# Performance work log

Hardware: AMD Instinct MI355X
Metric: run time of the kernel (lower is better)

## Reference

```python
import jax, jax.numpy as jnp
import numpy as np

H = 128   # hidden_size
IN = 4    # input_size
OUT = 4   # linear output dim


def _lstm_layer(x, Wih, Whh, bih, bhh):
    """Single PyTorch-convention LSTM layer (gate order i,f,g,o), batch_first.
    x: [B,T,D] -> hidden states [B,T,H]."""
    B, T, _ = x.shape
    Hd = Whh.shape[1]
    # Precompute input contribution to gates for all timesteps: [B,T,4H]
    xg = jnp.einsum('btd,gd->btg', x, Wih) + bih + bhh
    xg = jnp.swapaxes(xg, 0, 1)  # [T,B,4H] for scan
    h0 = jnp.zeros((B, Hd), x.dtype)
    c0 = jnp.zeros((B, Hd), x.dtype)

    def step(carry, gx):
        h, c = carry
        g = gx + h @ Whh.T            # [B,4H]
        i, f, gg, o = jnp.split(g, 4, axis=-1)
        i = jax.nn.sigmoid(i)
        f = jax.nn.sigmoid(f)
        gg = jnp.tanh(gg)
        o = jax.nn.sigmoid(o)
        c = f * c + i * gg
        h = o * jnp.tanh(c)
        return (h, c), h

    _, hs = jax.lax.scan(step, (h0, c0), xg)  # hs: [T,B,H]
    return jnp.swapaxes(hs, 0, 1)             # [B,T,H]


def setup_inputs() -> dict:
    key = jax.random.key(0)
    ks = jax.random.split(key, 11)
    B, T = 256, 2048
    s = 1.0 / np.sqrt(H)  # torch LSTM/Linear default init scale
    u = lambda k, shape: jax.random.uniform(k, shape, jnp.float32, -s, s)
    return dict(
        x=jax.random.normal(ks[0], (B, T, IN), jnp.float32),
        Wih0=u(ks[1], (4 * H, IN)),  Whh0=u(ks[2], (4 * H, H)),
        bih0=u(ks[3], (4 * H,)),     bhh0=u(ks[4], (4 * H,)),
        Wih1=u(ks[5], (4 * H, H)),   Whh1=u(ks[6], (4 * H, H)),
        bih1=u(ks[7], (4 * H,)),     bhh1=u(ks[8], (4 * H,)),
        Wlin=u(ks[9], (OUT, H)),     blin=u(ks[10], (OUT,)),
    )


def reference(x, Wih0, Whh0, bih0, bhh0, Wih1, Whh1, bih1, bhh1, Wlin, blin):
    h1 = _lstm_layer(x, Wih0, Whh0, bih0, bhh0)    # layer 0
    zs = _lstm_layer(h1, Wih1, Whh1, bih1, bhh1)   # layer 1, [B,T,H]
    z = zs[:, -1]                                  # last hidden state [B,H]
    v = jnp.einsum('bth,oh->bto', zs, Wlin) + blin # [B,T,4]
    return (v, z)
```

## Files before the change

### kernel.cpp

```cpp
#include <hip/hip_runtime.h>

#define BB 256
#define TT 2048
#define HH 128
#define HP 136
#define G4 512
#define INW 4
#define OUTW 4
#define TC 56
#define NT 512

typedef _Float16 f16x8 __attribute__((ext_vector_type(8)));
typedef float    f32x4 __attribute__((ext_vector_type(4)));

#define MFMA(A,B,C) __builtin_amdgcn_mfma_f32_16x16x32_f16((A),(B),(C),0,0,0)

__device__ __forceinline__ float sigm(float x)  { return __fdividef(1.f, 1.f + __expf(-x)); }
__device__ __forceinline__ float tanh_(float x) { return __fdividef(2.f, 1.f + __expf(-2.f*x)) - 1.f; }


#define LDF(dst, wrj, kk) do {                                                 \
    const float* p_ = Mp_ + (size_t)(wrj) * HH + (kk)*32 + (kq << 3);          \
    const float4 lo_ = *(const float4*)p_;                                     \
    const float4 hi_ = *(const float4*)(p_ + 4);                               \
    dst = (f16x8){(_Float16)lo_.x,(_Float16)lo_.y,(_Float16)lo_.z,             \
                  (_Float16)lo_.w,(_Float16)hi_.x,(_Float16)hi_.y,             \
                  (_Float16)hi_.z,(_Float16)hi_.w}; } while (0)

#define LOADW(M) do { const float* Mp_ = (M);                                  \
    LDF(w00, wr0,      0); LDF(w01, wr0,      1); LDF(w02, wr0,      2); LDF(w03, wr0,      3); \
    LDF(w10, wr0 + 4,  0); LDF(w11, wr0 + 4,  1); LDF(w12, wr0 + 4,  2); LDF(w13, wr0 + 4,  3); \
    LDF(w20, wr0 + 8,  0); LDF(w21, wr0 + 8,  1); LDF(w22, wr0 + 8,  2); LDF(w23, wr0 + 8,  3); \
    LDF(w30, wr0 + 12, 0); LDF(w31, wr0 + 12, 1); LDF(w32, wr0 + 12, 2); LDF(w33, wr0 + 12, 3); \
} while (0)

#define RSTEP(HB) do {                                                         \
    f16x8 hv_;                                                                 \
    hv_ = *(const f16x8*)((HB) + (kq << 3));                                   \
    a0 = MFMA(w00, hv_, a0); a1 = MFMA(w10, hv_, a1);                          \
    a2 = MFMA(w20, hv_, a2); a3 = MFMA(w30, hv_, a3);                          \
    hv_ = *(const f16x8*)((HB) + 32 + (kq << 3));                              \
    a0 = MFMA(w01, hv_, a0); a1 = MFMA(w11, hv_, a1);                          \
    a2 = MFMA(w21, hv_, a2); a3 = MFMA(w31, hv_, a3);                          \
    hv_ = *(const f16x8*)((HB) + 64 + (kq << 3));                              \
    a0 = MFMA(w02, hv_, a0); a1 = MFMA(w12, hv_, a1);                          \
    a2 = MFMA(w22, hv_, a2); a3 = MFMA(w32, hv_, a3);                          \
    hv_ = *(const f16x8*)((HB) + 96 + (kq << 3));                              \
    a0 = MFMA(w03, hv_, a0); a1 = MFMA(w13, hv_, a1);                          \
    a2 = MFMA(w23, hv_, a2); a3 = MFMA(w33, hv_, a3); } while (0)

#define UPDSEL(CJ, HN, XG) do {                                                \
    f32x4 av_;                                                                 \
    _Pragma("unroll")                                                          \
    for (int e_ = 0; e_ < 4; ++e_) {                                           \
        const float t01_ = j1 ? a1[e_] : a0[e_];                               \
        const float t23_ = j1 ? a3[e_] : a2[e_];                               \
        av_[e_] = (j2 ? t23_ : t01_) + (XG)[e_];                               \
    }                                                                          \
    const float i_ = sigm(av_[0]);                                             \
    const float f_ = sigm(av_[1]);                                             \
    const float g_ = tanh_(av_[2]);                                            \
    const float o_ = sigm(av_[3]);                                             \
    CJ = f_ * CJ + i_ * g_;                                                    \
    HN = o_ * tanh_(CJ); } while (0)

extern "C" __global__ void
__attribute__((amdgpu_flat_work_group_size(NT, NT)))
lstm2_fused(const float* __restrict__ x,
            const float* __restrict__ Wih0, const float* __restrict__ Whh0,
            const float* __restrict__ bih0, const float* __restrict__ bhh0,
            const float* __restrict__ Wih1, const float* __restrict__ Whh1,
            const float* __restrict__ bih1, const float* __restrict__ bhh1,
            const float* __restrict__ Wlin, const float* __restrict__ blin,
            float* __restrict__ out)
{
    __shared__ __align__(16) _Float16 h1h[(TC + 9) * HP];
    __shared__ __align__(16) float    buf[TC * G4];
    __shared__ __align__(16) _Float16 h2h[2 * HH];

    const int i    = threadIdx.x;
    const int w    = i >> 6;
    const int lane = i & 63;
    const int r    = lane & 15;
    const int kq   = lane >> 4;
    const int b    = blockIdx.x;

    const int wr0 = ((r & 3) << 7) | (r >> 2) | (w << 4);
    const bool j1 = (r & 1), j2 = (r & 2);
    const int  myu = (w << 4) | ((r & 3) << 2) | kq;
    const bool own = (r < 4);

    const int  rg_row = ((i & 3) << 7) | (i >> 2);
    const float4 wv   = *(const float4*)(Wih0 + (size_t)rg_row * INW);
    const float  b0r  = bih0[rg_row] + bhh0[rg_row];
    const float  bb0  = bih1[wr0]      + bhh1[wr0];
    const float  bb1  = bih1[wr0 + 4]  + bhh1[wr0 + 4];
    const float  bb2  = bih1[wr0 + 8]  + bhh1[wr0 + 8];
    const float  bb3  = bih1[wr0 + 12] + bhh1[wr0 + 12];
    const int   po = i >> 6;
    const int   pl = i & 63;
    const float wlA = (i < 256) ? Wlin[po * HH + pl]      : 0.f;
    const float wlB = (i < 256) ? Wlin[po * HH + 64 + pl] : 0.f;
    const float bl  = (i < 256) ? blin[po] : 0.f;

    if (i < HH) { h1h[i] = (_Float16)0.f; h2h[i] = (_Float16)0.f; }

    float c1 = 0.f, c2 = 0.f;
    f16x8 w00, w01, w02, w03, w10, w11, w12, w13,
          w20, w21, w22, w23, w30, w31, w32, w33;

    const float* xb   = x   + (size_t)b * TT * INW;
    float*       vout = out + (size_t)b * TT * OUTW;
    float*       zout = out + (size_t)BB * TT * OUTW + (size_t)b * HH;

    for (int t0 = 0; t0 < TT; t0 += TC) {
        const int tc = (TT - t0 < TC) ? (TT - t0) : TC;

        if (t0 > 0 && i < HH) h1h[i] = h1h[TC * HP + i];
        for (int t = 0; t < tc; ++t) {
            const float4 xv = *(const float4*)(xb + (size_t)(t0 + t) * INW);
            buf[t * G4 + i] = b0r + wv.x*xv.x + wv.y*xv.y + wv.z*xv.z + wv.w*xv.w;
        }
        LOADW(Whh0);
        __syncthreads();

        for (int t = 0; t < tc; ++t) {
            f32x4 a0 = {0.f,0.f,0.f,0.f}, a1 = {0.f,0.f,0.f,0.f},
                  a2 = {0.f,0.f,0.f,0.f}, a3 = {0.f,0.f,0.f,0.f};
            RSTEP(h1h + t * HP);
            const f32x4 xg = *(const f32x4*)(buf + t * G4 + (myu << 2));
            float hn;
            UPDSEL(c1, hn, xg);
            if (own) h1h[(t + 1) * HP + myu] = (_Float16)hn;
            __syncthreads();
        }

        LOADW(Wih1);
        const int ntb = (tc + 15) >> 4;
        for (int tb = 0; tb < ntb; ++tb) {
            f32x4 a0 = {0.f,0.f,0.f,0.f}, a1 = {0.f,0.f,0.f,0.f},
                  a2 = {0.f,0.f,0.f,0.f}, a3 = {0.f,0.f,0.f,0.f};
            const _Float16* ha = h1h + (tb * 16 + r + 1) * HP;
            f16x8 tv;
            tv = *(const f16x8*)(ha + (kq << 3));
            a0 = MFMA(tv, w00, a0); a1 = MFMA(tv, w10, a1);
            a2 = MFMA(tv, w20, a2); a3 = MFMA(tv, w30, a3);
            tv = *(const f16x8*)(ha + 32 + (kq << 3));
            a0 = MFMA(tv, w01, a0); a1 = MFMA(tv, w11, a1);
            a2 = MFMA(tv, w21, a2); a3 = MFMA(tv, w31, a3);
            tv = *(const f16x8*)(ha + 64 + (kq << 3));
            a0 = MFMA(tv, w02, a0); a1 = MFMA(tv, w12, a1);
            a2 = MFMA(tv, w22, a2); a3 = MFMA(tv, w32, a3);
            tv = *(const f16x8*)(ha + 96 + (kq << 3));
            a0 = MFMA(tv, w03, a0); a1 = MFMA(tv, w13, a1);
            a2 = MFMA(tv, w23, a2); a3 = MFMA(tv, w33, a3);
            #pragma unroll
            for (int e = 0; e < 4; ++e) {
                const int tl = tb * 16 + (kq << 2) + e;
                if (tl < tc) {
                    float* bq = buf + tl * G4 + (w << 6) + r;
                    bq[0]  = a0[e] + bb0;
                    bq[16] = a1[e] + bb1;
                    bq[32] = a2[e] + bb2;
                    bq[48] = a3[e] + bb3;
                }
            }
        }
        __syncthreads();

        LOADW(Whh1);
        for (int t = 0; t < tc; ++t) {
            const int rb = (t & 1) * HH, wbuf = rb ^ HH;
            f32x4 a0 = {0.f,0.f,0.f,0.f}, a1 = {0.f,0.f,0.f,0.f},
                  a2 = {0.f,0.f,0.f,0.f}, a3 = {0.f,0.f,0.f,0.f};
            RSTEP(h2h + rb);
            const f32x4 xg = *(const f32x4*)(buf + t * G4 + (myu << 2));
            float hn;
            UPDSEL(c2, hn, xg);
            if (own) {
                h2h[wbuf + myu] = (_Float16)hn;
                if (t0 + t == TT - 1) zout[myu] = hn;
            }
            __syncthreads();
            if (i < 256) {
                float p2 = (float)h2h[wbuf + pl] * wlA
                         + (float)h2h[wbuf + 64 + pl] * wlB;
                p2 += __shfl_xor(p2, 32);
                p2 += __shfl_xor(p2, 16);
                p2 += __shfl_xor(p2, 8);
                p2 += __shfl_xor(p2, 4);
                p2 += __shfl_xor(p2, 2);
                p2 += __shfl_xor(p2, 1);
                if (pl == 0) vout[(size_t)(t0 + t) * OUTW + po] = p2 + bl;
            }
        }
    }
}

extern "C" void kernel_launch(void* const* d_in, const int* in_sizes, int n_in,
                              void* d_out, int out_size, void* d_ws, size_t ws_size,
                              hipStream_t stream) {
    const float* x    = (const float*)d_in[0];
    const float* Wih0 = (const float*)d_in[1];
    const float* Whh0 = (const float*)d_in[2];
    const float* bih0 = (const float*)d_in[3];
    const float* bhh0 = (const float*)d_in[4];
    const float* Wih1 = (const float*)d_in[5];
    const float* Whh1 = (const float*)d_in[6];
    const float* bih1 = (const float*)d_in[7];
    const float* bhh1 = (const float*)d_in[8];
    const float* Wlin = (const float*)d_in[9];
    const float* blin = (const float*)d_in[10];
    float* out = (float*)d_out;

    lstm2_fused<<<dim3(BB), dim3(NT), 0, stream>>>(
        x, Wih0, Whh0, bih0, bhh0, Wih1, Whh1, bih1, bhh1, Wlin, blin, out);
}
```

Before: 3.161 ms.

## Pipeline LSTM layers across paired producer/consumer blocks via global-memory flags

Splits each batch row across two workgroups: one runs layer 0's recurrence and writes chunks of hidden states to a global ring of slots, and the other consumes them to run layer 1's input GEMM, its recurrence and the output projection. Chunks are handed off with release/acquire flags and generation tags, so the two layers' serial recurrences overlap instead of running back to back. Workgroups shrink to 256 threads, each wave now computes 8 gate tiles, and the layer-0 input projection is computed inline per step. The cost is spin-waiting, slot traffic through global memory, and a dependence on both blocks of a pair being resident at once, otherwise it can deadlock.

New measurement: 4.317 ms. +36.6%, slower.

```diff
diff --git a/kernel.cpp b/kernel.cpp
--- a/kernel.cpp
+++ b/kernel.cpp
@@ -1,14 +1,14 @@
 #include <hip/hip_runtime.h>
 
-#define BB 256
-#define TT 2048
-#define HH 128
-#define HP 136
-#define G4 512
-#define INW 4
+#define BB   256
+#define TT   2048
+#define HH   128
+#define G4   512
+#define INW  4
 #define OUTW 4
-#define TC 56
-#define NT 512
+#define TC   32
+#define NCH  64
+#define NT   256
 
 typedef _Float16 f16x8 __attribute__((ext_vector_type(8)));
 typedef float    f32x4 __attribute__((ext_vector_type(4)));
@@ -27,35 +27,45 @@
                   (_Float16)lo_.w,(_Float16)hi_.x,(_Float16)hi_.y,             \
                   (_Float16)hi_.z,(_Float16)hi_.w}; } while (0)
 
-#define LOADW(M) do { const float* Mp_ = (M);                                  \
+#define LOADW8(M) do { const float* Mp_ = (M);                                 \
     LDF(w00, wr0,      0); LDF(w01, wr0,      1); LDF(w02, wr0,      2); LDF(w03, wr0,      3); \
     LDF(w10, wr0 + 4,  0); LDF(w11, wr0 + 4,  1); LDF(w12, wr0 + 4,  2); LDF(w13, wr0 + 4,  3); \
     LDF(w20, wr0 + 8,  0); LDF(w21, wr0 + 8,  1); LDF(w22, wr0 + 8,  2); LDF(w23, wr0 + 8,  3); \
     LDF(w30, wr0 + 12, 0); LDF(w31, wr0 + 12, 1); LDF(w32, wr0 + 12, 2); LDF(w33, wr0 + 12, 3); \
+    LDF(w40, wr0 + 16, 0); LDF(w41, wr0 + 16, 1); LDF(w42, wr0 + 16, 2); LDF(w43, wr0 + 16, 3); \
+    LDF(w50, wr0 + 20, 0); LDF(w51, wr0 + 20, 1); LDF(w52, wr0 + 20, 2); LDF(w53, wr0 + 20, 3); \
+    LDF(w60, wr0 + 24, 0); LDF(w61, wr0 + 24, 1); LDF(w62, wr0 + 24, 2); LDF(w63, wr0 + 24, 3); \
+    LDF(w70, wr0 + 28, 0); LDF(w71, wr0 + 28, 1); LDF(w72, wr0 + 28, 2); LDF(w73, wr0 + 28, 3); \
 } while (0)
 
-#define RSTEP(HB) do {                                                         \
-    f16x8 hv_;                                                                 \
-    hv_ = *(const f16x8*)((HB) + (kq << 3));                                   \
-    a0 = MFMA(w00, hv_, a0); a1 = MFMA(w10, hv_, a1);                          \
-    a2 = MFMA(w20, hv_, a2); a3 = MFMA(w30, hv_, a3);                          \
-    hv_ = *(const f16x8*)((HB) + 32 + (kq << 3));                              \
-    a0 = MFMA(w01, hv_, a0); a1 = MFMA(w11, hv_, a1);                          \
-    a2 = MFMA(w21, hv_, a2); a3 = MFMA(w31, hv_, a3);                          \
-    hv_ = *(const f16x8*)((HB) + 64 + (kq << 3));                              \
-    a0 = MFMA(w02, hv_, a0); a1 = MFMA(w12, hv_, a1);                          \
-    a2 = MFMA(w22, hv_, a2); a3 = MFMA(w32, hv_, a3);                          \
-    hv_ = *(const f16x8*)((HB) + 96 + (kq << 3));                              \
-    a0 = MFMA(w03, hv_, a0); a1 = MFMA(w13, hv_, a1);                          \
-    a2 = MFMA(w23, hv_, a2); a3 = MFMA(w33, hv_, a3); } while (0)
-
-#define UPDSEL(CJ, HN, XG) do {                                                \
+#define RS1(kk, OFS) do {                                                      \
+    const f16x8 hv_ = *(const f16x8*)(HB_ + (OFS) + (kq << 3));                \
+    a0 = MFMA(w0##kk, hv_, a0); a1 = MFMA(w1##kk, hv_, a1);                    \
+    a2 = MFMA(w2##kk, hv_, a2); a3 = MFMA(w3##kk, hv_, a3);                    \
+    a4 = MFMA(w4##kk, hv_, a4); a5 = MFMA(w5##kk, hv_, a5);                    \
+    a6 = MFMA(w6##kk, hv_, a6); a7 = MFMA(w7##kk, hv_, a7); } while (0)
+
+#define RSTEP8(HBP) do { const _Float16* HB_ = (HBP);                          \
+    RS1(0, 0); RS1(1, 32); RS1(2, 64); RS1(3, 96); } while (0)
+
+#define BS1(kk) do {                                                           \
+    const f16x8 tv_ = *(const f16x8*)(ar_ + (kk)*32 + (kq << 3));              \
+    a0 = MFMA(tv_, w0##kk, a0); a1 = MFMA(tv_, w1##kk, a1);                    \
+    a2 = MFMA(tv_, w2##kk, a2); a3 = MFMA(tv_, w3##kk, a3);                    \
+    a4 = MFMA(tv_, w4##kk, a4); a5 = MFMA(tv_, w5##kk, a5);                    \
+    a6 = MFMA(tv_, w6##kk, a6); a7 = MFMA(tv_, w7##kk, a7); } while (0)
+
+#define UPDSEL8(CJ, HN, XG) do {                                               \
     f32x4 av_;                                                                 \
     _Pragma("unroll")                                                          \
     for (int e_ = 0; e_ < 4; ++e_) {                                           \
-        const float t01_ = j1 ? a1[e_] : a0[e_];                               \
-        const float t23_ = j1 ? a3[e_] : a2[e_];                               \
-        av_[e_] = (j2 ? t23_ : t01_) + (XG)[e_];                               \
+        const float s01_ = j1b ? a1[e_] : a0[e_];                              \
+        const float s23_ = j1b ? a3[e_] : a2[e_];                              \
+        const float s45_ = j1b ? a5[e_] : a4[e_];                              \
+        const float s67_ = j1b ? a7[e_] : a6[e_];                              \
+        const float sA_ = j2b ? s23_ : s01_;                                   \
+        const float sB_ = j2b ? s67_ : s45_;                                   \
+        av_[e_] = (j4b ? sB_ : sA_) + (XG)[e_];                                \
     }                                                                          \
     const float i_ = sigm(av_[0]);                                             \
     const float f_ = sigm(av_[1]);                                             \
@@ -64,135 +74,193 @@
     CJ = f_ * CJ + i_ * g_;                                                    \
     HN = o_ * tanh_(CJ); } while (0)
 
+#define PROJ(OFS, VT) do {                                                     \
+    float p2_ = (float)h2h[(OFS) + pl] * wlA                                   \
+              + (float)h2h[(OFS) + 64 + pl] * wlB;                             \
+    p2_ += __shfl_xor(p2_, 32);                                                \
+    p2_ += __shfl_xor(p2_, 16);                                                \
+    p2_ += __shfl_xor(p2_, 8);                                                 \
+    p2_ += __shfl_xor(p2_, 4);                                                 \
+    p2_ += __shfl_xor(p2_, 2);                                                 \
+    p2_ += __shfl_xor(p2_, 1);                                                 \
+    if (pl == 0) vbuf[(VT) * OUTW + po] = p2_ + bl; } while (0)
+
+#define TAG(C) (((g) << 7) | (unsigned)((C) + 1))
+
 extern "C" __global__ void
 __attribute__((amdgpu_flat_work_group_size(NT, NT)))
-lstm2_fused(const float* __restrict__ x,
-            const float* __restrict__ Wih0, const float* __restrict__ Whh0,
-            const float* __restrict__ bih0, const float* __restrict__ bhh0,
-            const float* __restrict__ Wih1, const float* __restrict__ Whh1,
-            const float* __restrict__ bih1, const float* __restrict__ bhh1,
-            const float* __restrict__ Wlin, const float* __restrict__ blin,
-            float* __restrict__ out)
+lstm2_pipe(const float* __restrict__ x,
+           const float* __restrict__ Wih0, const float* __restrict__ Whh0,
+           const float* __restrict__ bih0, const float* __restrict__ bhh0,
+           const float* __restrict__ Wih1, const float* __restrict__ Whh1,
+           const float* __restrict__ bih1, const float* __restrict__ bhh1,
+           const float* __restrict__ Wlin, const float* __restrict__ blin,
+           float* __restrict__ out,
+           unsigned* __restrict__ genPair, unsigned* __restrict__ flagsA,
+           unsigned* __restrict__ doneA, _Float16* __restrict__ slots, int S)
 {
-    __shared__ __align__(16) _Float16 h1h[(TC + 9) * HP];
-    __shared__ __align__(16) float    buf[TC * G4];
+    __shared__ __align__(16) _Float16 ring[(TC + 1) * HH];
+    __shared__ __align__(16) float    xgbuf[TC * G4];
     __shared__ __align__(16) _Float16 h2h[2 * HH];
+    __shared__ __align__(16) float    vbuf[TC * OUTW];
+    __shared__ unsigned gshare;
 
     const int i    = threadIdx.x;
     const int w    = i >> 6;
     const int lane = i & 63;
     const int r    = lane & 15;
     const int kq   = lane >> 4;
-    const int b    = blockIdx.x;
-
-    const int wr0 = ((r & 3) << 7) | (r >> 2) | (w << 4);
-    const bool j1 = (r & 1), j2 = (r & 2);
-    const int  myu = (w << 4) | ((r & 3) << 2) | kq;
-    const bool own = (r < 4);
-
-    const int  rg_row = ((i & 3) << 7) | (i >> 2);
-    const float4 wv   = *(const float4*)(Wih0 + (size_t)rg_row * INW);
-    const float  b0r  = bih0[rg_row] + bhh0[rg_row];
-    const float  bb0  = bih1[wr0]      + bhh1[wr0];
-    const float  bb1  = bih1[wr0 + 4]  + bhh1[wr0 + 4];
-    const float  bb2  = bih1[wr0 + 8]  + bhh1[wr0 + 8];
-    const float  bb3  = bih1[wr0 + 12] + bhh1[wr0 + 12];
-    const int   po = i >> 6;
-    const int   pl = i & 63;
-    const float wlA = (i < 256) ? Wlin[po * HH + pl]      : 0.f;
-    const float wlB = (i < 256) ? Wlin[po * HH + 64 + pl] : 0.f;
-    const float bl  = (i < 256) ? blin[po] : 0.f;
-
-    if (i < HH) { h1h[i] = (_Float16)0.f; h2h[i] = (_Float16)0.f; }
-
-    float c1 = 0.f, c2 = 0.f;
-    f16x8 w00, w01, w02, w03, w10, w11, w12, w13,
-          w20, w21, w22, w23, w30, w31, w32, w33;
-
-    const float* xb   = x   + (size_t)b * TT * INW;
-    float*       vout = out + (size_t)b * TT * OUTW;
-    float*       zout = out + (size_t)BB * TT * OUTW + (size_t)b * HH;
-
-    for (int t0 = 0; t0 < TT; t0 += TC) {
-        const int tc = (TT - t0 < TC) ? (TT - t0) : TC;
-
-        if (t0 > 0 && i < HH) h1h[i] = h1h[TC * HP + i];
-        for (int t = 0; t < tc; ++t) {
-            const float4 xv = *(const float4*)(xb + (size_t)(t0 + t) * INW);
-            buf[t * G4 + i] = b0r + wv.x*xv.x + wv.y*xv.y + wv.z*xv.z + wv.w*xv.w;
+    const int bp   = blockIdx.x >> 1;
+    const int role = blockIdx.x & 1;
+
+    const int wr0 = ((r & 3) << 7) | (w << 5) | (r >> 2);
+    const bool j1b = (r & 1), j2b = (r & 2), j4b = (r & 4);
+    const int  u   = (w << 5) | ((r & 7) << 2) | kq;
+    const bool own = (r < 8);
+
+    if (i == 0)
+        gshare = __hip_atomic_fetch_add(&genPair[bp], 1u, __ATOMIC_RELAXED,
+                                        __HIP_MEMORY_SCOPE_AGENT) >> 1;
+    __syncthreads();
+    const unsigned g = gshare;
+
+    unsigned* myflag = flagsA + bp * NCH;
+    unsigned* mydone = doneA  + bp * NCH;
+    _Float16* myslot0 = slots + (size_t)bp * S * (TC * HH);
+
+    f16x8 w00,w01,w02,w03, w10,w11,w12,w13, w20,w21,w22,w23, w30,w31,w32,w33,
+          w40,w41,w42,w43, w50,w51,w52,w53, w60,w61,w62,w63, w70,w71,w72,w73;
+
+    if (role == 0) {
+        const float* xb = x + (size_t)bp * TT * INW;
+        const float4 wxa = *(const float4*)(Wih0 + (size_t)u * INW);
+        const float4 wxb = *(const float4*)(Wih0 + (size_t)(128 + u) * INW);
+        const float4 wxc = *(const float4*)(Wih0 + (size_t)(256 + u) * INW);
+        const float4 wxd = *(const float4*)(Wih0 + (size_t)(384 + u) * INW);
+        const float b0a = bih0[u]       + bhh0[u];
+        const float b0b = bih0[128 + u] + bhh0[128 + u];
+        const float b0c = bih0[256 + u] + bhh0[256 + u];
+        const float b0d = bih0[384 + u] + bhh0[384 + u];
+        LOADW8(Whh0);
+        if (i < HH) ring[i] = (_Float16)0.f;
+        float c1 = 0.f;
+        __syncthreads();
+
+        for (int c = 0; c < NCH; ++c) {
+            const int t0 = c * TC;
+            if (c >= S) {
+                if (i == 0) {
+                    const unsigned exp_ = TAG(c - S);
+                    while (__hip_atomic_load(&mydone[c - S], __ATOMIC_RELAXED,
+                                             __HIP_MEMORY_SCOPE_AGENT) != exp_)
+                        __builtin_amdgcn_s_sleep(8);
+                }
+                __syncthreads();
+                __builtin_amdgcn_fence(__ATOMIC_ACQUIRE, "agent");
+            }
+            if (c > 0) {
+                if (i < HH) ring[i] = ring[TC * HH + i];
+                __syncthreads();
+            }
+            for (int t = 0; t < TC; ++t) {
+                f32x4 a0={0,0,0,0},a1={0,0,0,0},a2={0,0,0,0},a3={0,0,0,0},
+                      a4={0,0,0,0},a5={0,0,0,0},a6={0,0,0,0},a7={0,0,0,0};
+                RSTEP8(ring + t * HH);
+                const float4 xv = *(const float4*)(xb + (size_t)(t0 + t) * INW);
+                f32x4 xg;
+                xg[0] = b0a + wxa.x*xv.x + wxa.y*xv.y + wxa.z*xv.z + wxa.w*xv.w;
+                xg[1] = b0b + wxb.x*xv.x + wxb.y*xv.y + wxb.z*xv.z + wxb.w*xv.w;
+                xg[2] = b0c + wxc.x*xv.x + wxc.y*xv.y + wxc.z*xv.z + wxc.w*xv.w;
+                xg[3] = b0d + wxd.x*xv.x + wxd.y*xv.y + wxd.z*xv.z + wxd.w*xv.w;
+                float hn;
+                UPDSEL8(c1, hn, xg);
+                if (own) ring[(t + 1) * HH + u] = (_Float16)hn;
+                __syncthreads();
+            }
+            {
+                unsigned* dst = (unsigned*)(myslot0 + (size_t)(c % S) * (TC * HH));
+                const unsigned* src = (const unsigned*)(ring + HH);
+                for (int jj = i; jj < TC * HH / 2; jj += NT) dst[jj] = src[jj];
+            }
+            __builtin_amdgcn_fence(__ATOMIC_RELEASE, "agent");
+            __syncthreads();
+            if (i == 0)
+                __hip_atomic_store(&myflag[c], TAG(c), __ATOMIC_RELEASE,
+                                   __HIP_MEMORY_SCOPE_AGENT);
         }
-        LOADW(Whh0);
+    } else {
+        float* vout = out + (size_t)bp * TT * OUTW;
+        float* zout = out + (size_t)BB * TT * OUTW + (size_t)bp * HH;
+        const float bb0 = bih1[wr0]      + bhh1[wr0];
+        const float bb1 = bih1[wr0 + 4]  + bhh1[wr0 + 4];
+        const float bb2 = bih1[wr0 + 8]  + bhh1[wr0 + 8];
+        const float bb3 = bih1[wr0 + 12] + bhh1[wr0 + 12];
+        const float bb4 = bih1[wr0 + 16] + bhh1[wr0 + 16];
+        const float bb5 = bih1[wr0 + 20] + bhh1[wr0 + 20];
+        const float bb6 = bih1[wr0 + 24] + bhh1[wr0 + 24];
+        const float bb7 = bih1[wr0 + 28] + bhh1[wr0 + 28];
+        const int   po = i >> 6;
+        const int   pl = i & 63;
+        const float wlA = Wlin[po * HH + pl];
+        const float wlB = Wlin[po * HH + 64 + pl];
+        const float bl  = blin[po];
+        if (i < HH) h2h[i] = (_Float16)0.f;
+        float c2 = 0.f;
         __syncthreads();
 
-        for (int t = 0; t < tc; ++t) {
-            f32x4 a0 = {0.f,0.f,0.f,0.f}, a1 = {0.f,0.f,0.f,0.f},
-                  a2 = {0.f,0.f,0.f,0.f}, a3 = {0.f,0.f,0.f,0.f};
-            RSTEP(h1h + t * HP);
-            const f32x4 xg = *(const f32x4*)(buf + t * G4 + (myu << 2));
-            float hn;
-            UPDSEL(c1, hn, xg);
-            if (own) h1h[(t + 1) * HP + myu] = (_Float16)hn;
-            __syncthreads();
-        }
-
-        LOADW(Wih1);
-        const int ntb = (tc + 15) >> 4;
-        for (int tb = 0; tb < ntb; ++tb) {
-            f32x4 a0 = {0.f,0.f,0.f,0.f}, a1 = {0.f,0.f,0.f,0.f},
-                  a2 = {0.f,0.f,0.f,0.f}, a3 = {0.f,0.f,0.f,0.f};
-            const _Float16* ha = h1h + (tb * 16 + r + 1) * HP;
-            f16x8 tv;
-            tv = *(const f16x8*)(ha + (kq << 3));
-            a0 = MFMA(tv, w00, a0); a1 = MFMA(tv, w10, a1);
-            a2 = MFMA(tv, w20, a2); a3 = MFMA(tv, w30, a3);
-            tv = *(const f16x8*)(ha + 32 + (kq << 3));
-            a0 = MFMA(tv, w01, a0); a1 = MFMA(tv, w11, a1);
-            a2 = MFMA(tv, w21, a2); a3 = MFMA(tv, w31, a3);
-            tv = *(const f16x8*)(ha + 64 + (kq << 3));
-            a0 = MFMA(tv, w02, a0); a1 = MFMA(tv, w12, a1);
-            a2 = MFMA(tv, w22, a2); a3 = MFMA(tv, w32, a3);
-            tv = *(const f16x8*)(ha + 96 + (kq << 3));
-            a0 = MFMA(tv, w03, a0); a1 = MFMA(tv, w13, a1);
-            a2 = MFMA(tv, w23, a2); a3 = MFMA(tv, w33, a3);
-            #pragma unroll
-            for (int e = 0; e < 4; ++e) {
-                const int tl = tb * 16 + (kq << 2) + e;
-                if (tl < tc) {
-                    float* bq = buf + tl * G4 + (w << 6) + r;
-                    bq[0]  = a0[e] + bb0;
-                    bq[16] = a1[e] + bb1;
-                    bq[32] = a2[e] + bb2;
-                    bq[48] = a3[e] + bb3;
+        for (int c = 0; c < NCH; ++c) {
+            const int t0 = c * TC;
+            LOADW8(Wih1);
+            if (i == 0) {
+                const unsigned exp_ = TAG(c);
+                while (__hip_atomic_load(&myflag[c], __ATOMIC_RELAXED,
+                                         __HIP_MEMORY_SCOPE_AGENT) != exp_)
+                    __builtin_amdgcn_s_sleep(8);
+            }
+            __syncthreads();
+            __builtin_amdgcn_fence(__ATOMIC_ACQUIRE, "agent");
+            const _Float16* sc = myslot0 + (size_t)(c % S) * (TC * HH);
+
+            for (int tb = 0; tb < TC / 16; ++tb) {
+                f32x4 a0={0,0,0,0},a1={0,0,0,0},a2={0,0,0,0},a3={0,0,0,0},
+                      a4={0,0,0,0},a5={0,0,0,0},a6={0,0,0,0},a7={0,0,0,0};
+                const _Float16* ar_ = sc + (size_t)(tb * 16 + r) * HH;
+                BS1(0); BS1(1); BS1(2); BS1(3);
+                #pragma unroll
+                for (int e = 0; e < 4; ++e) {
+                    const int tl = tb * 16 + (kq << 2) + e;
+                    float* bq = xgbuf + tl * G4 + (w << 7) + r;
+                    bq[0]   = a0[e] + bb0;  bq[16]  = a1[e] + bb1;
+                    bq[32]  = a2[e] + bb2;  bq[48]  = a3[e] + bb3;
+                    bq[64]  = a4[e] + bb4;  bq[80]  = a5[e] + bb5;
+                    bq[96]  = a6[e] + bb6;  bq[112] = a7[e] + bb7;
                 }
             }
-        }
-        __syncthreads();
-
-        LOADW(Whh1);
-        for (int t = 0; t < tc; ++t) {
-            const int rb = (t & 1) * HH, wbuf = rb ^ HH;
-            f32x4 a0 = {0.f,0.f,0.f,0.f}, a1 = {0.f,0.f,0.f,0.f},
-                  a2 = {0.f,0.f,0.f,0.f}, a3 = {0.f,0.f,0.f,0.f};
-            RSTEP(h2h + rb);
-            const f32x4 xg = *(const f32x4*)(buf + t * G4 + (myu << 2));
-            float hn;
-            UPDSEL(c2, hn, xg);
-            if (own) {
-                h2h[wbuf + myu] = (_Float16)hn;
-                if (t0 + t == TT - 1) zout[myu] = hn;
-            }
-            __syncthreads();
-            if (i < 256) {
-                float p2 = (float)h2h[wbuf + pl] * wlA
-                         + (float)h2h[wbuf + 64 + pl] * wlB;
-                p2 += __shfl_xor(p2, 32);
-                p2 += __shfl_xor(p2, 16);
-                p2 += __shfl_xor(p2, 8);
-                p2 += __shfl_xor(p2, 4);
-                p2 += __shfl_xor(p2, 2);
-                p2 += __shfl_xor(p2, 1);
-                if (pl == 0) vout[(size_t)(t0 + t) * OUTW + po] = p2 + bl;
-            }
+            __syncthreads();
+            if (i == 0)
+                __hip_atomic_store(&mydone[c], TAG(c), __ATOMIC_RELEASE,
+                                   __HIP_MEMORY_SCOPE_AGENT);
+            LOADW8(Whh1);
+
+            for (int t = 0; t < TC; ++t) {
+                const int rb = (t & 1) * HH, wb2 = rb ^ HH;
+                f32x4 a0={0,0,0,0},a1={0,0,0,0},a2={0,0,0,0},a3={0,0,0,0},
+                      a4={0,0,0,0},a5={0,0,0,0},a6={0,0,0,0},a7={0,0,0,0};
+                RSTEP8(h2h + rb);
+                if (t > 0) PROJ(rb, t - 1);
+                const f32x4 xg = *(const f32x4*)(xgbuf + t * G4 + (u << 2));
+                float hn;
+                UPDSEL8(c2, hn, xg);
+                if (own) {
+                    h2h[wb2 + u] = (_Float16)hn;
+                    if (t0 + t == TT - 1) zout[u] = hn;
+                }
+                __syncthreads();
+            }
+            PROJ(0, TC - 1);
+            __syncthreads();
+            for (int jj = i; jj < TC * OUTW; jj += NT)
+                vout[(size_t)t0 * OUTW + jj] = vbuf[jj];
         }
     }
 }
@@ -213,6 +281,19 @@
     const float* blin = (const float*)d_in[10];
     float* out = (float*)d_out;
 
-    lstm2_fused<<<dim3(BB), dim3(NT), 0, stream>>>(
-        x, Wih0, Whh0, bih0, bhh0, Wih1, Whh1, bih1, bhh1, Wlin, blin, out);
+    unsigned* wsu     = (unsigned*)d_ws;
+    unsigned* genPair = wsu;
+    unsigned* flagsA  = wsu + BB;
+    unsigned* doneA   = flagsA + BB * NCH;
+    const size_t hdr_u = (size_t)BB + 2u * BB * NCH;
+    _Float16* slots = (_Float16*)(wsu + hdr_u);
+    const size_t slot_halfs = (size_t)TC * HH;
+    long long avail = ((long long)ws_size - (long long)(hdr_u * 4)) / 2;
+    int S = (avail > 0) ? (int)(avail / (long long)(BB * slot_halfs)) : 1;
+    if (S < 1) S = 1;
+    if (S > NCH) S = NCH;
+
+    lstm2_pipe<<<dim3(2 * BB), dim3(NT), 0, stream>>>(
+        x, Wih0, Whh0, bih0, bhh0, Wih1, Whh1, bih1, bhh1, Wlin, blin, out,
+        genPair, flagsA, doneA, slots, S);
 }
```
